# Kernel tuning notes

Measured on AMD Instinct MI355X. Metric: run time of the kernel, lower is better.

Reference implementation:

```python
import jax, jax.numpy as jnp
import numpy as np

N, E, G = 50000, 300000, 64
VOCAB, EMB, FEAT = 10000, 64, 8
DIN, DH, EDIM = EMB * FEAT, 256, 6


def _lin(k, fout, fin):
    kw, kb = jax.random.split(k)
    w = jax.random.normal(kw, (fout, fin), jnp.float32) / float(np.sqrt(fin))
    b = jax.random.normal(kb, (fout,), jnp.float32) * 0.01
    return w, b


def setup_inputs() -> dict:
    key = jax.random.key(0)
    ks = jax.random.split(key, 10)
    inp = {
        'x_idx': jax.random.randint(ks[0], (N, FEAT), 0, VOCAB),
        'edge_index': jax.random.randint(ks[1], (2, E), 0, N),
        'edge_attr': jax.random.normal(ks[2], (E, EDIM), jnp.float32),
        'batch': jnp.sort(jax.random.randint(ks[3], (N,), 0, G)),
        'emb_table': jax.random.normal(ks[4], (VOCAB, EMB), jnp.float32) * 0.1,
    }
    # two TransformerConv layers: lin_query/key/value (d_in->DH), lin_edge (EDIM->DH), lin_skip (d_in->DH)
    for li, kbase, din in ((1, ks[5], DIN), (2, ks[6], DH)):
        sub = jax.random.split(kbase, 5)
        for j, (wn, bn, fin) in enumerate([('wq', 'bq', din), ('wk', 'bk', din), ('wv', 'bv', din), ('we', 'be', EDIM), ('ws', 'bs', din)]):
            w, b = _lin(sub[j], DH, fin)
            inp['c%d_%s' % (li, wn)] = w
            inp['c%d_%s' % (li, bn)] = b
    for i, (fout, fin, k) in enumerate([(256, 2 * DH, ks[7]), (128, 256, ks[8]), (1, 128, ks[9])]):
        w, b = _lin(k, fout, fin)
        inp['w%d' % (i + 1)] = w
        inp['b%d' % (i + 1)] = b
    return inp


def _tconv(h, src, dst, edge_attr, wq, bq, wk, bk, wv, bv, we, be, ws, bs):
    # PyG TransformerConv, heads=1, concat=True, root_weight=True, beta=False
    n = h.shape[0]
    q = h @ wq.T + bq                      # [N, DH]
    k = h @ wk.T + bk
    v = h @ wv.T + bv
    e = edge_attr @ we.T + be              # [E, DH]
    ke = k[src] + e                        # key fused with edge features
    logits = jnp.sum(q[dst] * ke, axis=-1) / jnp.sqrt(jnp.float32(DH))  # [E]
    m = jax.ops.segment_max(logits, dst, num_segments=n)
    m = jnp.where(jnp.isfinite(m), m, 0.0)
    a = jnp.exp(logits - m[dst])
    s = jax.ops.segment_sum(a, dst, num_segments=n)
    a = a / s[dst]                         # scatter-softmax over incoming edges
    agg = jax.ops.segment_sum((v[src] + e) * a[:, None], dst, num_segments=n)
    return agg + h @ ws.T + bs             # skip connection (root_weight)


def reference(x_idx, edge_index, edge_attr, batch, emb_table,
              c1_wq, c1_bq, c1_wk, c1_bk, c1_wv, c1_bv, c1_we, c1_be, c1_ws, c1_bs,
              c2_wq, c2_bq, c2_wk, c2_bk, c2_wv, c2_bv, c2_we, c2_be, c2_ws, c2_bs,
              w1, b1, w2, b2, w3, b3):
    x = emb_table[x_idx].reshape(x_idx.shape[0], DIN)  # [N, EMB*FEAT]
    src, dst = edge_index[0], edge_index[1]
    h = jax.nn.relu(_tconv(x, src, dst, edge_attr, c1_wq, c1_bq, c1_wk, c1_bk, c1_wv, c1_bv, c1_we, c1_be, c1_ws, c1_bs))
    h = jax.nn.relu(_tconv(h, src, dst, edge_attr, c2_wq, c2_bq, c2_wk, c2_bk, c2_wv, c2_bv, c2_we, c2_be, c2_ws, c2_bs))
    cnt = jax.ops.segment_sum(jnp.ones((h.shape[0],), h.dtype), batch, num_segments=G)
    gap = jax.ops.segment_sum(h, batch, num_segments=G) / jnp.maximum(cnt, 1.0)[:, None]
    gmp = jax.ops.segment_max(h, batch, num_segments=G)
    gmp = jnp.where(jnp.isfinite(gmp), gmp, 0.0)
    r = jnp.concatenate([gap, gmp], axis=1)             # [G, 2*DH]
    o = jax.nn.relu(r @ w1.T + b1)
    o = jax.nn.relu(o @ w2.T + b2)
    # dropout skipped (eval mode)
    return jax.nn.sigmoid(o @ w3.T + b3)[:, 0]          # [G]
```

## Files before the change

kernel.cpp:

```cpp
#include <hip/hip_runtime.h>

typedef unsigned long long ull;
typedef __bf16 bf16x8 __attribute__((ext_vector_type(8)));
typedef float f32x4 __attribute__((ext_vector_type(4)));

__device__ __forceinline__ float bf2f(unsigned short u) {
  union { unsigned int i; float f; } c; c.i = ((unsigned int)u) << 16; return c.f;
}
__device__ __forceinline__ unsigned short f2bf(float f) {
  union { float f; unsigned int i; } c; c.f = f;
  unsigned int u = c.i;
  u += 0x7fffu + ((u >> 16) & 1u);
  return (unsigned short)(u >> 16);
}

__global__ __launch_bounds__(256) void pack_weights(
    const float* __restrict__ wq, const float* __restrict__ wk,
    const float* __restrict__ wv, const float* __restrict__ ws,
    const float* __restrict__ bq, const float* __restrict__ bk,
    const float* __restrict__ bv, const float* __restrict__ bs,
    unsigned short* __restrict__ Wcat, float* __restrict__ bcat, int logK) {
  int idx = blockIdx.x * 256 + threadIdx.x;
  if (idx < 1024) {
    int rr = idx >> 8, cc = idx & 255;
    const float* bp = (rr == 0) ? bq : (rr == 1) ? bk : (rr == 2) ? bv : bs;
    bcat[idx] = bp[cc];
  }
  int K = 1 << logK;
  if (idx >= (1024 << logK)) return;
  int kj = idx & 7;
  int lane = (idx >> 3) & 63;
  int rg = (idx >> 9) & 3;
  int ksbits = logK - 5;
  int ks = (idx >> 11) & ((1 << ksbits) - 1);
  int colt = idx >> (11 + ksbits);
  int quad = lane >> 4, lm = lane & 15;
  int o = colt * 64 + rg * 16 + lm;
  int k = ks * 32 + quad * 8 + kj;
  int rr = o >> 8, oo = o & 255;
  const float* wp = (rr == 0) ? wq : (rr == 1) ? wk : (rr == 2) ? wv : ws;
  Wcat[idx] = f2bf(wp[oo * K + k]);
}

__global__ __launch_bounds__(256) void embed_gather(
    const int* __restrict__ x_idx, const float* __restrict__ emb,
    unsigned short* __restrict__ xbf, int total) {
  int idx = blockIdx.x * 256 + threadIdx.x;
  if (idx >= total) return;
  int n = idx >> 9, d = idx & 511, f = d >> 6, j = d & 63;
  int vi = x_idx[n * 8 + f];
  int n32 = n >> 5, lm = n & 15, half = (n >> 4) & 1;
  int ks = d >> 5, quad = (d >> 3) & 3, kj = d & 7;
  size_t a = (((size_t)(n32 * 16 + ks)) * 2 + half) * 512 + (quad * 16 + lm) * 8 + kj;
  xbf[a] = f2bf(emb[vi * 64 + j]);
}

__global__ __launch_bounds__(256) void count_dst(const int* __restrict__ dst,
                                                 int* __restrict__ counts, int E_) {
  int i = blockIdx.x * 256 + threadIdx.x;
  if (i < E_) atomicAdd(&counts[dst[i]], 1);
}

__global__ __launch_bounds__(256) void alloc_rows(const int* __restrict__ counts,
                                                  int* __restrict__ row_start,
                                                  int* __restrict__ cursor,
                                                  int* __restrict__ total, int n) {
  int i = blockIdx.x * 256 + threadIdx.x;
  int lane = threadIdx.x & 63;
  int c = (i < n) ? counts[i] : 0;
  int incl = c;
#pragma unroll
  for (int off = 1; off < 64; off <<= 1) {
    int t = __shfl_up(incl, off, 64);
    if (lane >= off) incl += t;
  }
  int base = 0;
  if (lane == 63) base = atomicAdd(total, incl);
  base = __shfl(base, 63, 64);
  int st = base + incl - c;
  if (i < n) { row_start[i] = st; cursor[i] = st; }
}

__global__ __launch_bounds__(256) void scatter_edges(
    const int* __restrict__ dst, const int* __restrict__ srcA,
    const float* __restrict__ eattr, int* __restrict__ cursor,
    int* __restrict__ srcs, int* __restrict__ dsts,
    float* __restrict__ ea_perm, int E_) {
  int i = blockIdx.x * 256 + threadIdx.x;
  if (i >= E_) return;
  int d = dst[i];
  int p = atomicAdd(&cursor[d], 1);
  srcs[p] = srcA[i];
  dsts[p] = d;
  const float* ea = eattr + (size_t)i * 6;
  float* eo = ea_perm + (size_t)p * 6;
  eo[0] = ea[0]; eo[1] = ea[1]; eo[2] = ea[2];
  eo[3] = ea[3]; eo[4] = ea[4]; eo[5] = ea[5];
}

template <int K>
__global__ __launch_bounds__(256) void gemm_qkvs(
    const unsigned short* __restrict__ X, const unsigned short* __restrict__ W,
    const float* __restrict__ bcat,
    unsigned short* __restrict__ qout, unsigned short* __restrict__ kout,
    unsigned short* __restrict__ vout, float* __restrict__ sout,
    int Nn, int nrb) {
  const int l = blockIdx.x;
  const int xcd = l & 7, j = l >> 3;
  const int q = nrb >> 3, r = nrb & 7;
  const int cnt = q + (xcd < r ? 1 : 0);
  const int lrb = j >> 4, colt = j & 15;
  if (lrb >= cnt) return;
  const int m_blk = xcd * q + min(xcd, r) + lrb;

  const int wid = threadIdx.x >> 6;
  const int lane = threadIdx.x & 63;
  const int quad = lane >> 4, lm = lane & 15;
  const int m_base = m_blk * 128 + wid * 32;
  const int n_base = colt * 64;
  const size_t abase = (size_t)(m_blk * 4 + wid) * (K >> 5) * 1024 + lane * 8;
  const size_t bbase = (size_t)colt * (K >> 5) * 2048 + lane * 8;
  f32x4 acc[2][4] = {};
#pragma unroll 4
  for (int ks = 0; ks < (K >> 5); ks++) {
    const unsigned short* ap = X + abase + (size_t)ks * 1024;
    const unsigned short* bp = W + bbase + (size_t)ks * 2048;
    bf16x8 a0 = *(const bf16x8*)(ap);
    bf16x8 a1 = *(const bf16x8*)(ap + 512);
    bf16x8 b0 = *(const bf16x8*)(bp);
    bf16x8 b1 = *(const bf16x8*)(bp + 512);
    bf16x8 b2 = *(const bf16x8*)(bp + 1024);
    bf16x8 b3 = *(const bf16x8*)(bp + 1536);
    acc[0][0] = __builtin_amdgcn_mfma_f32_16x16x32_bf16(a0, b0, acc[0][0], 0, 0, 0);
    acc[0][1] = __builtin_amdgcn_mfma_f32_16x16x32_bf16(a0, b1, acc[0][1], 0, 0, 0);
    acc[0][2] = __builtin_amdgcn_mfma_f32_16x16x32_bf16(a0, b2, acc[0][2], 0, 0, 0);
    acc[0][3] = __builtin_amdgcn_mfma_f32_16x16x32_bf16(a0, b3, acc[0][3], 0, 0, 0);
    acc[1][0] = __builtin_amdgcn_mfma_f32_16x16x32_bf16(a1, b0, acc[1][0], 0, 0, 0);
    acc[1][1] = __builtin_amdgcn_mfma_f32_16x16x32_bf16(a1, b1, acc[1][1], 0, 0, 0);
    acc[1][2] = __builtin_amdgcn_mfma_f32_16x16x32_bf16(a1, b2, acc[1][2], 0, 0, 0);
    acc[1][3] = __builtin_amdgcn_mfma_f32_16x16x32_bf16(a1, b3, acc[1][3], 0, 0, 0);
  }
#pragma unroll
  for (int mi = 0; mi < 2; mi++) {
#pragma unroll
    for (int r2 = 0; r2 < 4; r2++) {
      int row = m_base + mi * 16 + quad * 4 + r2;
      if (row >= Nn) continue;
      size_t rb = (size_t)row * 256;
#pragma unroll
      for (int ni = 0; ni < 4; ni++) {
        int col = n_base + ni * 16 + lm;
        float v = acc[mi][ni][r2] + bcat[col];
        int reg = col >> 8, c = col & 255;
        if (reg == 0)       qout[rb + c] = f2bf(v * 0.0625f);
        else if (reg == 1)  kout[rb + c] = f2bf(v);
        else if (reg == 2)  vout[rb + c] = f2bf(v);
        else                sout[rb + c] = v;
      }
    }
  }
}

__global__ __launch_bounds__(256) void node_prep(
    const unsigned short* __restrict__ qv,
    const float* __restrict__ we, const float* __restrict__ be,
    float* __restrict__ zc, int Nn) {
  __shared__ float we_s[1536];
  __shared__ float be_s[256];
  for (int i = threadIdx.x; i < 1536; i += 256) we_s[i] = we[i];
  be_s[threadIdx.x] = be[threadIdx.x];
  __syncthreads();
  int wid = threadIdx.x >> 6, lane = threadIdx.x & 63;
  int n = blockIdx.x * 4 + wid;
  if (n >= Nn) return;
  int j0 = lane * 4;
  ull uq = *(const ull*)(qv + (size_t)n * 256 + j0);
  float q0 = bf2f((unsigned short)uq), q1 = bf2f((unsigned short)(uq >> 16));
  float q2 = bf2f((unsigned short)(uq >> 32)), q3 = bf2f((unsigned short)(uq >> 48));
  float part[7];
#pragma unroll
  for (int t = 0; t < 6; t++) {
    part[t] = we_s[(j0 + 0) * 6 + t] * q0 + we_s[(j0 + 1) * 6 + t] * q1
            + we_s[(j0 + 2) * 6 + t] * q2 + we_s[(j0 + 3) * 6 + t] * q3;
  }
  part[6] = be_s[j0] * q0 + be_s[j0 + 1] * q1 + be_s[j0 + 2] * q2 + be_s[j0 + 3] * q3;
#pragma unroll
  for (int off = 32; off > 0; off >>= 1) {
#pragma unroll
    for (int t = 0; t < 7; t++) part[t] += __shfl_xor(part[t], off, 64);
  }
  if (lane == 0) {
    float* zp = zc + (size_t)n * 8;
#pragma unroll
    for (int t = 0; t < 7; t++) zp[t] = part[t];
    zp[7] = 0.f;
  }
}

__device__ __forceinline__ float dot4(ull uq, ull uk) {
  return bf2f((unsigned short)uq) * bf2f((unsigned short)uk)
       + bf2f((unsigned short)(uq >> 16)) * bf2f((unsigned short)(uk >> 16))
       + bf2f((unsigned short)(uq >> 32)) * bf2f((unsigned short)(uk >> 32))
       + bf2f((unsigned short)(uq >> 48)) * bf2f((unsigned short)(uk >> 48));
}

#define SEL8_I(a, t) ((t)==0?(a)[0]:(t)==1?(a)[1]:(t)==2?(a)[2]:(t)==3?(a)[3]:(t)==4?(a)[4]:(t)==5?(a)[5]:(t)==6?(a)[6]:(a)[7])

__global__ __launch_bounds__(256) void edge_logits(
    const int* __restrict__ srcs, const int* __restrict__ dsts,
    const float* __restrict__ ea_perm,
    const unsigned short* __restrict__ qv, const unsigned short* __restrict__ kv,
    const float* __restrict__ zc, int E_, float* __restrict__ logits) {
  int wid = threadIdx.x >> 6, lane = threadIdx.x & 63;
  int p0 = (blockIdx.x * 4 + wid) * 8;
  if (p0 >= E_) return;
  int j0 = lane * 4;
  int s_[8], d_[8];
  if (p0 + 8 <= E_) {
    int4 sa = *(const int4*)(srcs + p0), sb = *(const int4*)(srcs + p0 + 4);
    int4 da = *(const int4*)(dsts + p0), db = *(const int4*)(dsts + p0 + 4);
    s_[0] = sa.x; s_[1] = sa.y; s_[2] = sa.z; s_[3] = sa.w;
    s_[4] = sb.x; s_[5] = sb.y; s_[6] = sb.z; s_[7] = sb.w;
    d_[0] = da.x; d_[1] = da.y; d_[2] = da.z; d_[3] = da.w;
    d_[4] = db.x; d_[5] = db.y; d_[6] = db.z; d_[7] = db.w;
  } else {
#pragma unroll
    for (int t = 0; t < 8; t++) {
      int pp = min(p0 + t, E_ - 1);
      s_[t] = srcs[pp]; d_[t] = dsts[pp];
    }
  }
  ull uk[8], uq[8];
#pragma unroll
  for (int t = 0; t < 8; t++) uk[t] = *(const ull*)(kv + (size_t)s_[t] * 256 + j0);
#pragma unroll
  for (int t = 0; t < 8; t++) uq[t] = *(const ull*)(qv + (size_t)d_[t] * 256 + j0);
  float pv[8];
#pragma unroll
  for (int t = 0; t < 8; t++) pv[t] = dot4(uq[t], uk[t]);
#pragma unroll
  for (int off = 32; off > 0; off >>= 1) {
#pragma unroll
    for (int t = 0; t < 8; t++) pv[t] += __shfl_xor(pv[t], off, 64);
  }
  if (lane < 8 && p0 + lane < E_) {
    int t = lane;
    int dd = SEL8_I(d_, t);
    float pvt = SEL8_I(pv, t);
    const float* zp = zc + (size_t)dd * 8;
    const float* u = ea_perm + (size_t)(p0 + t) * 6;
    float zd = zp[0] * u[0] + zp[1] * u[1] + zp[2] * u[2]
             + zp[3] * u[3] + zp[4] * u[4] + zp[5] * u[5] + zp[6];
    logits[p0 + t] = pvt + zd;
  }
}

__global__ __launch_bounds__(256) void node_softmax(
    const int* __restrict__ row_start, const int* __restrict__ counts,
    const float* __restrict__ ea_perm,
    float* __restrict__ logits, float* __restrict__ ubar, int Nn) {
  int wid = threadIdx.x >> 6, lane = threadIdx.x & 63;
  int n = blockIdx.x * 4 + wid;
  if (n >= Nn) return;
  int beg = row_start[n], cnt = counts[n];
  if (cnt == 0) return;
  float lm = -INFINITY;
  for (int b = lane; b < cnt; b += 64) lm = fmaxf(lm, logits[beg + b]);
#pragma unroll
  for (int off = 32; off > 0; off >>= 1) lm = fmaxf(lm, __shfl_xor(lm, off, 64));
  float se = 0.f;
  for (int b = lane; b < cnt; b += 64) se += __expf(logits[beg + b] - lm);
#pragma unroll
  for (int off = 32; off > 0; off >>= 1) se += __shfl_xor(se, off, 64);
  float inv = 1.f / se;
  float u0 = 0.f, u1 = 0.f, u2 = 0.f, u3 = 0.f, u4 = 0.f, u5 = 0.f;
  for (int b = lane; b < cnt; b += 64) {
    int p = beg + b;
    float w = __expf(logits[p] - lm) * inv;
    logits[p] = w;
    const float* up = ea_perm + (size_t)p * 6;
    u0 += w * up[0]; u1 += w * up[1]; u2 += w * up[2];
    u3 += w * up[3]; u4 += w * up[4]; u5 += w * up[5];
  }
#pragma unroll
  for (int off = 32; off > 0; off >>= 1) {
    u0 += __shfl_xor(u0, off, 64); u1 += __shfl_xor(u1, off, 64);
    u2 += __shfl_xor(u2, off, 64); u3 += __shfl_xor(u3, off, 64);
    u4 += __shfl_xor(u4, off, 64); u5 += __shfl_xor(u5, off, 64);
  }
  if (lane == 0) {
    float* up = ubar + (size_t)n * 8;
    up[0] = u0; up[1] = u1; up[2] = u2; up[3] = u3; up[4] = u4; up[5] = u5;
  }
}

#define NPW 8
__global__ __launch_bounds__(256) void edge_agg_final(
    const int* __restrict__ srcs, const int* __restrict__ row_start,
    const int* __restrict__ counts, const float* __restrict__ wgt,
    const unsigned short* __restrict__ vv,
    const float* __restrict__ ubar, const float* __restrict__ skipv,
    const float* __restrict__ we, const float* __restrict__ be,
    int Nn, int mode,
    unsigned short* __restrict__ hout, float* __restrict__ h_acc) {
  __shared__ float we_s[1536];
  __shared__ float be_s[256];
  for (int i = threadIdx.x; i < 1536; i += 256) we_s[i] = we[i];
  be_s[threadIdx.x] = be[threadIdx.x];
  __syncthreads();
  int wave = blockIdx.x * 4 + (threadIdx.x >> 6);
  int lane = threadIdx.x & 63;
  int n0 = wave * NPW;
  if (n0 >= Nn) return;
  int n1 = min(n0 + NPW, Nn);
  int j0 = lane * 4;
  for (int n = n0; n < n1; n++) {
    int cnt = counts[n];
    float a0 = 0.f, a1 = 0.f, a2 = 0.f, a3 = 0.f;
    float e[4] = {0.f, 0.f, 0.f, 0.f};
    if (cnt > 0) {
      int beg = row_start[n];
      for (int i0 = 0; i0 < cnt; i0 += 8) {
        int m = cnt - i0; if (m > 8) m = 8;
        float w8[8];
        int s8[8];
#pragma unroll
        for (int t = 0; t < 8; t++) {
          int pp = beg + i0 + ((t < m) ? t : (m - 1));
          w8[t] = (t < m) ? wgt[pp] : 0.f;
          s8[t] = srcs[pp];
        }
        ull uv[8];
#pragma unroll
        for (int t = 0; t < 8; t++)
          uv[t] = *(const ull*)(vv + (size_t)s8[t] * 256 + j0);
#pragma unroll
        for (int t = 0; t < 8; t++) {
          float ww = w8[t];
          a0 += ww * bf2f((unsigned short)uv[t]);
          a1 += ww * bf2f((unsigned short)(uv[t] >> 16));
          a2 += ww * bf2f((unsigned short)(uv[t] >> 32));
          a3 += ww * bf2f((unsigned short)(uv[t] >> 48));
        }
      }
      float4 u0 = *(const float4*)(ubar + (size_t)n * 8);
      float4 u1 = *(const float4*)(ubar + (size_t)n * 8 + 4);
#pragma unroll
      for (int r = 0; r < 4; r++) {
        int d = j0 + r;
        e[r] = be_s[d]
             + we_s[d * 6 + 0] * u0.x + we_s[d * 6 + 1] * u0.y + we_s[d * 6 + 2] * u0.z
             + we_s[d * 6 + 3] * u0.w + we_s[d * 6 + 4] * u1.x + we_s[d * 6 + 5] * u1.y;
      }
    }
    float4 skv = *(const float4*)(skipv + (size_t)n * 256 + j0);
    float h0 = fmaxf(a0 + e[0] + skv.x, 0.f);
    float h1 = fmaxf(a1 + e[1] + skv.y, 0.f);
    float h2 = fmaxf(a2 + e[2] + skv.z, 0.f);
    float h3 = fmaxf(a3 + e[3] + skv.w, 0.f);
    if (mode == 0) {
      ull hv = (ull)f2bf(h0) | ((ull)f2bf(h1) << 16) | ((ull)f2bf(h2) << 32) | ((ull)f2bf(h3) << 48);
      int n32 = n >> 5, lmn = n & 15, halfn = (n >> 4) & 1;
      int ks = lane >> 3, quadc = (lane >> 1) & 3, kjc = (lane & 1) * 4;
      size_t a = (((size_t)(n32 * 8 + ks)) * 2 + halfn) * 512 + (quadc * 16 + lmn) * 8 + kjc;
      *(ull*)(hout + a) = hv;
    } else {
      float4 o; o.x = h0; o.y = h1; o.z = h2; o.w = h3;
      *(float4*)(h_acc + (size_t)n * 256 + j0) = o;
    }
  }
}

__global__ __launch_bounds__(256) void pool_reduce(
    const float* __restrict__ hfin, const int* __restrict__ batch, int Nn,
    float* __restrict__ gap, unsigned int* __restrict__ gmp) {
  int g = blockIdx.x, s = blockIdx.y, t = threadIdx.x;
  __shared__ int st_s, en_s;
  if (t == 0) {
    int lo = 0, hi = Nn;
    while (lo < hi) { int mid = (lo + hi) >> 1; if (batch[mid] < g) lo = mid + 1; else hi = mid; }
    st_s = lo;
    lo = 0; hi = Nn;
    while (lo < hi) { int mid = (lo + hi) >> 1; if (batch[mid] < g + 1) lo = mid + 1; else hi = mid; }
    en_s = lo;
  }
  __syncthreads();
  int st = st_s, en = en_s;
  int len = en - st;
  if (len <= 0) return;
  int nsplit = gridDim.y;
  int chunk = (len + nsplit - 1) / nsplit;
  int a = st + s * chunk;
  int b = min(a + chunk, en);
  if (a >= b) return;
  float acc = 0.f, mx = 0.f;
  for (int n = a; n < b; n++) {
    float v = hfin[(size_t)n * 256 + t];
    acc += v;
    mx = fmaxf(mx, v);
  }
  atomicAdd(&gap[(size_t)g * 256 + t], acc);
  atomicMax(&gmp[(size_t)g * 256 + t], __float_as_uint(mx));
}

__global__ __launch_bounds__(256) void pool_mlp(
    const float* __restrict__ gap, const unsigned int* __restrict__ gmp,
    const int* __restrict__ batch, int Nn,
    const float* __restrict__ w1, const float* __restrict__ b1,
    const float* __restrict__ w2, const float* __restrict__ b2,
    const float* __restrict__ w3, const float* __restrict__ b3,
    float* __restrict__ out) {
  int g = blockIdx.x, t = threadIdx.x;
  __shared__ float r[512];
  __shared__ float o1[256];
  __shared__ float o2[128];
  __shared__ float red[256];
  __shared__ int cnt_s;
  if (t == 0) {
    int lo = 0, hi = Nn;
    while (lo < hi) { int mid = (lo + hi) >> 1; if (batch[mid] < g) lo = mid + 1; else hi = mid; }
    int st = lo;
    lo = 0; hi = Nn;
    while (lo < hi) { int mid = (lo + hi) >> 1; if (batch[mid] < g + 1) lo = mid + 1; else hi = mid; }
    cnt_s = lo - st;
  }
  __syncthreads();
  float inv = 1.f / fmaxf((float)cnt_s, 1.f);
  r[t] = gap[(size_t)g * 256 + t] * inv;
  r[256 + t] = __uint_as_float(gmp[(size_t)g * 256 + t]);
  __syncthreads();
  {
    float a = b1[t];
    const float* wr = w1 + (size_t)t * 512;
    for (int k = 0; k < 512; k++) a += wr[k] * r[k];
    o1[t] = fmaxf(a, 0.f);
  }
  __syncthreads();
  if (t < 128) {
    float a = b2[t];
    const float* wr = w2 + (size_t)t * 256;
    for (int k = 0; k < 256; k++) a += wr[k] * o1[k];
    o2[t] = fmaxf(a, 0.f);
  }
  __syncthreads();
  red[t] = (t < 128) ? w3[t] * o2[t] : 0.f;
  __syncthreads();
  for (int s = 128; s > 0; s >>= 1) {
    if (t < s) red[t] += red[t + s];
    __syncthreads();
  }
  if (t == 0) out[g] = 1.f / (1.f + expf(-(red[0] + b3[0])));
}

extern "C" void kernel_launch(void* const* d_in, const int* in_sizes, int n_in,
                              void* d_out, int out_size, void* d_ws, size_t ws_size,
                              hipStream_t stream) {
  const int* x_idx      = (const int*)d_in[0];
  const int* edge_index = (const int*)d_in[1];
  const float* eattr    = (const float*)d_in[2];
  const int* batch      = (const int*)d_in[3];
  const float* emb      = (const float*)d_in[4];
  const float* c1_wq = (const float*)d_in[5],  *c1_bq = (const float*)d_in[6];
  const float* c1_wk = (const float*)d_in[7],  *c1_bk = (const float*)d_in[8];
  const float* c1_wv = (const float*)d_in[9],  *c1_bv = (const float*)d_in[10];
  const float* c1_we = (const float*)d_in[11], *c1_be = (const float*)d_in[12];
  const float* c1_ws = (const float*)d_in[13], *c1_bs = (const float*)d_in[14];
  const float* c2_wq = (const float*)d_in[15], *c2_bq = (const float*)d_in[16];
  const float* c2_wk = (const float*)d_in[17], *c2_bk = (const float*)d_in[18];
  const float* c2_wv = (const float*)d_in[19], *c2_bv = (const float*)d_in[20];
  const float* c2_we = (const float*)d_in[21], *c2_be = (const float*)d_in[22];
  const float* c2_ws = (const float*)d_in[23], *c2_bs = (const float*)d_in[24];
  const float* w1 = (const float*)d_in[25], *b1 = (const float*)d_in[26];
  const float* w2 = (const float*)d_in[27], *b2 = (const float*)d_in[28];
  const float* w3 = (const float*)d_in[29], *b3 = (const float*)d_in[30];

  const int Nn = in_sizes[3];
  const int Ee = in_sizes[1] / 2;
  const int nrb = (Nn + 127) / 128;

  char* ws = (char*)d_ws;
  size_t off = 0;
  auto alloc = [&](size_t bytes) -> void* {
    void* p = ws + off;
    off += (bytes + 255) & ~(size_t)255;
    return p;
  };
  unsigned short* xbf   = (unsigned short*)alloc((size_t)nrb * 128 * 512 * 2);
  unsigned short* qbf   = (unsigned short*)alloc((size_t)Nn * 256 * 2);
  unsigned short* kbf   = (unsigned short*)alloc((size_t)Nn * 256 * 2);
  unsigned short* vbf   = (unsigned short*)alloc((size_t)Nn * 256 * 2);
  float*          skipf = (float*)alloc((size_t)Nn * 256 * 4);
  unsigned short* h1bf  = (unsigned short*)alloc((size_t)nrb * 128 * 256 * 2);
  unsigned short* Wcat1 = (unsigned short*)alloc((size_t)1024 * 512 * 2);
  float*          bcat1 = (float*)alloc(1024 * 4);
  unsigned short* Wcat2 = (unsigned short*)alloc((size_t)1024 * 256 * 2);
  float*          bcat2 = (float*)alloc(1024 * 4);
  int*            counts    = (int*)alloc((size_t)Nn * 4);
  int*            row_start = (int*)alloc((size_t)Nn * 4);
  int*            cursor    = (int*)alloc((size_t)Nn * 4);
  int*            srcs      = (int*)alloc((size_t)Ee * 4);
  int*            dsts      = (int*)alloc((size_t)Ee * 4);
  float*          ea_perm   = (float*)alloc((size_t)Ee * 6 * 4);
  float*          logits    = (float*)alloc((size_t)Ee * 4);
  float*          zc        = (float*)alloc((size_t)Nn * 8 * 4);
  float*          ubar      = (float*)alloc((size_t)Nn * 8 * 4);
  int*            total     = (int*)alloc(256);
  float*          gap       = (float*)alloc((size_t)64 * 256 * 4);
  unsigned int*   gmp       = (unsigned int*)alloc((size_t)64 * 256 * 4);
  float* h_acc = (float*)xbf;

  const int* srcA = edge_index;
  const int* dstA = edge_index + Ee;

  hipMemsetAsync(counts, 0, (size_t)Nn * 4, stream);
  hipMemsetAsync(total, 0, 4, stream);
  hipMemsetAsync(gap, 0, (size_t)64 * 256 * 4, stream);
  hipMemsetAsync(gmp, 0, (size_t)64 * 256 * 4, stream);

  pack_weights<<<(1024 * 512 + 255) / 256, 256, 0, stream>>>(
      c1_wq, c1_wk, c1_wv, c1_ws, c1_bq, c1_bk, c1_bv, c1_bs, Wcat1, bcat1, 9);
  pack_weights<<<(1024 * 256 + 255) / 256, 256, 0, stream>>>(
      c2_wq, c2_wk, c2_wv, c2_ws, c2_bq, c2_bk, c2_bv, c2_bs, Wcat2, bcat2, 8);
  embed_gather<<<((Nn * 512) + 255) / 256, 256, 0, stream>>>(x_idx, emb, xbf, Nn * 512);
  count_dst<<<(Ee + 255) / 256, 256, 0, stream>>>(dstA, counts, Ee);
  alloc_rows<<<(Nn + 255) / 256, 256, 0, stream>>>(counts, row_start, cursor, total, Nn);
  scatter_edges<<<(Ee + 255) / 256, 256, 0, stream>>>(dstA, srcA, eattr, cursor,
                                                      srcs, dsts, ea_perm, Ee);

  const int rbmax = nrb / 8 + ((nrb % 8) ? 1 : 0);
  const int ggrid = 8 * rbmax * 16;
  const int egrid = (Ee + 31) / 32;
  const int sgrid = (Nn + NPW * 4 - 1) / (NPW * 4);
  const int ngrid = (Nn + 3) / 4;

  gemm_qkvs<512><<<ggrid, 256, 0, stream>>>(xbf, Wcat1, bcat1, qbf, kbf, vbf,
                                            skipf, Nn, nrb);
  node_prep<<<ngrid, 256, 0, stream>>>(qbf, c1_we, c1_be, zc, Nn);
  edge_logits<<<egrid, 256, 0, stream>>>(srcs, dsts, ea_perm, qbf, kbf, zc, Ee, logits);
  node_softmax<<<ngrid, 256, 0, stream>>>(row_start, counts, ea_perm, logits, ubar, Nn);
  edge_agg_final<<<sgrid, 256, 0, stream>>>(srcs, row_start, counts, logits, vbf,
                                            ubar, skipf, c1_we, c1_be, Nn, 0,
                                            h1bf, nullptr);

  gemm_qkvs<256><<<ggrid, 256, 0, stream>>>(h1bf, Wcat2, bcat2, qbf, kbf, vbf,
                                            skipf, Nn, nrb);
  node_prep<<<ngrid, 256, 0, stream>>>(qbf, c2_we, c2_be, zc, Nn);
  edge_logits<<<egrid, 256, 0, stream>>>(srcs, dsts, ea_perm, qbf, kbf, zc, Ee, logits);
  node_softmax<<<ngrid, 256, 0, stream>>>(row_start, counts, ea_perm, logits, ubar, Nn);
  edge_agg_final<<<sgrid, 256, 0, stream>>>(srcs, row_start, counts, logits, vbf,
                                            ubar, skipf, c2_we, c2_be, Nn, 1,
                                            nullptr, h_acc);

  dim3 pg(64, 16);
  pool_reduce<<<pg, 256, 0, stream>>>(h_acc, batch, Nn, gap, gmp);
  pool_mlp<<<64, 256, 0, stream>>>(gap, gmp, batch, Nn, w1, b1, w2, b2, w3, b3,
                                   (float*)d_out);
}
```

Before: 768.8 us.

## Stage GEMM weight tiles in double-buffered LDS shared by all waves

The QKVS projection GEMM now loads each weight tile into a double-buffered shared-memory buffer once per block, instead of having each of the four waves read it from global memory separately. The load of the next chunk of four k-steps is issued before the MFMAs on the current chunk and written to the other buffer afterwards, so global loads overlap with compute. This cuts redundant global and L2 traffic for the weight operand. In exchange it adds 32 KB of LDS per block, which may lower occupancy, plus a block-wide barrier per chunk. The activation operand is still read straight from global memory.

```diff
diff --git a/kernel.cpp b/kernel.cpp
--- a/kernel.cpp
+++ b/kernel.cpp
@@ -105,6 +105,7 @@
     unsigned short* __restrict__ qout, unsigned short* __restrict__ kout,
     unsigned short* __restrict__ vout, float* __restrict__ sout,
     int Nn, int nrb) {
+  __shared__ unsigned short Bs[2][8192];
   const int l = blockIdx.x;
   const int xcd = l & 7, j = l >> 3;
   const int q = nrb >> 3, r = nrb & 7;
@@ -113,32 +114,68 @@
   if (lrb >= cnt) return;
   const int m_blk = xcd * q + min(xcd, r) + lrb;
 
-  const int wid = threadIdx.x >> 6;
-  const int lane = threadIdx.x & 63;
+  const int tid = threadIdx.x;
+  const int wid = tid >> 6;
+  const int lane = tid & 63;
   const int quad = lane >> 4, lm = lane & 15;
   const int m_base = m_blk * 128 + wid * 32;
   const int n_base = colt * 64;
   const size_t abase = (size_t)(m_blk * 4 + wid) * (K >> 5) * 1024 + lane * 8;
-  const size_t bbase = (size_t)colt * (K >> 5) * 2048 + lane * 8;
+  const unsigned short* wchunk = W + (size_t)colt * (K >> 5) * 2048;
+  const int nc = (K >> 5) / 4;
   f32x4 acc[2][4] = {};
-#pragma unroll 4
-  for (int ks = 0; ks < (K >> 5); ks++) {
-    const unsigned short* ap = X + abase + (size_t)ks * 1024;
-    const unsigned short* bp = W + bbase + (size_t)ks * 2048;
-    bf16x8 a0 = *(const bf16x8*)(ap);
-    bf16x8 a1 = *(const bf16x8*)(ap + 512);
-    bf16x8 b0 = *(const bf16x8*)(bp);
-    bf16x8 b1 = *(const bf16x8*)(bp + 512);
-    bf16x8 b2 = *(const bf16x8*)(bp + 1024);
-    bf16x8 b3 = *(const bf16x8*)(bp + 1536);
-    acc[0][0] = __builtin_amdgcn_mfma_f32_16x16x32_bf16(a0, b0, acc[0][0], 0, 0, 0);
-    acc[0][1] = __builtin_amdgcn_mfma_f32_16x16x32_bf16(a0, b1, acc[0][1], 0, 0, 0);
-    acc[0][2] = __builtin_amdgcn_mfma_f32_16x16x32_bf16(a0, b2, acc[0][2], 0, 0, 0);
-    acc[0][3] = __builtin_amdgcn_mfma_f32_16x16x32_bf16(a0, b3, acc[0][3], 0, 0, 0);
-    acc[1][0] = __builtin_amdgcn_mfma_f32_16x16x32_bf16(a1, b0, acc[1][0], 0, 0, 0);
-    acc[1][1] = __builtin_amdgcn_mfma_f32_16x16x32_bf16(a1, b1, acc[1][1], 0, 0, 0);
-    acc[1][2] = __builtin_amdgcn_mfma_f32_16x16x32_bf16(a1, b2, acc[1][2], 0, 0, 0);
-    acc[1][3] = __builtin_amdgcn_mfma_f32_16x16x32_bf16(a1, b3, acc[1][3], 0, 0, 0);
+
+  {
+    bf16x8 st0 = *(const bf16x8*)(wchunk + 0 * 2048 + tid * 8);
+    bf16x8 st1 = *(const bf16x8*)(wchunk + 1 * 2048 + tid * 8);
+    bf16x8 st2 = *(const bf16x8*)(wchunk + 2 * 2048 + tid * 8);
+    bf16x8 st3 = *(const bf16x8*)(wchunk + 3 * 2048 + tid * 8);
+    *(bf16x8*)(&Bs[0][0 * 2048 + tid * 8]) = st0;
+    *(bf16x8*)(&Bs[0][1 * 2048 + tid * 8]) = st1;
+    *(bf16x8*)(&Bs[0][2 * 2048 + tid * 8]) = st2;
+    *(bf16x8*)(&Bs[0][3 * 2048 + tid * 8]) = st3;
+  }
+  __syncthreads();
+
+  for (int c = 0; c < nc; c++) {
+    bf16x8 st0, st1, st2, st3;
+    const bool pf = (c + 1 < nc);
+    if (pf) {
+      const unsigned short* wp = wchunk + (size_t)(c + 1) * 8192;
+      st0 = *(const bf16x8*)(wp + 0 * 2048 + tid * 8);
+      st1 = *(const bf16x8*)(wp + 1 * 2048 + tid * 8);
+      st2 = *(const bf16x8*)(wp + 2 * 2048 + tid * 8);
+      st3 = *(const bf16x8*)(wp + 3 * 2048 + tid * 8);
+    }
+    const unsigned short* bs = &Bs[c & 1][0];
+#pragma unroll
+    for (int s = 0; s < 4; s++) {
+      const int ks = c * 4 + s;
+      const unsigned short* ap = X + abase + (size_t)ks * 1024;
+      const unsigned short* bp = bs + s * 2048 + lane * 8;
+      bf16x8 a0 = *(const bf16x8*)(ap);
+      bf16x8 a1 = *(const bf16x8*)(ap + 512);
+      bf16x8 b0 = *(const bf16x8*)(bp);
+      bf16x8 b1 = *(const bf16x8*)(bp + 512);
+      bf16x8 b2 = *(const bf16x8*)(bp + 1024);
+      bf16x8 b3 = *(const bf16x8*)(bp + 1536);
+      acc[0][0] = __builtin_amdgcn_mfma_f32_16x16x32_bf16(a0, b0, acc[0][0], 0, 0, 0);
+      acc[0][1] = __builtin_amdgcn_mfma_f32_16x16x32_bf16(a0, b1, acc[0][1], 0, 0, 0);
+      acc[0][2] = __builtin_amdgcn_mfma_f32_16x16x32_bf16(a0, b2, acc[0][2], 0, 0, 0);
+      acc[0][3] = __builtin_amdgcn_mfma_f32_16x16x32_bf16(a0, b3, acc[0][3], 0, 0, 0);
+      acc[1][0] = __builtin_amdgcn_mfma_f32_16x16x32_bf16(a1, b0, acc[1][0], 0, 0, 0);
+      acc[1][1] = __builtin_amdgcn_mfma_f32_16x16x32_bf16(a1, b1, acc[1][1], 0, 0, 0);
+      acc[1][2] = __builtin_amdgcn_mfma_f32_16x16x32_bf16(a1, b2, acc[1][2], 0, 0, 0);
+      acc[1][3] = __builtin_amdgcn_mfma_f32_16x16x32_bf16(a1, b3, acc[1][3], 0, 0, 0);
+    }
+    if (pf) {
+      unsigned short* bw = &Bs[(c + 1) & 1][0];
+      *(bf16x8*)(bw + 0 * 2048 + tid * 8) = st0;
+      *(bf16x8*)(bw + 1 * 2048 + tid * 8) = st1;
+      *(bf16x8*)(bw + 2 * 2048 + tid * 8) = st2;
+      *(bf16x8*)(bw + 3 * 2048 + tid * 8) = st3;
+    }
+    __syncthreads();
   }
 #pragma unroll
   for (int mi = 0; mi < 2; mi++) {
@@ -151,11 +188,11 @@
       for (int ni = 0; ni < 4; ni++) {
         int col = n_base + ni * 16 + lm;
         float v = acc[mi][ni][r2] + bcat[col];
-        int reg = col >> 8, c = col & 255;
-        if (reg == 0)       qout[rb + c] = f2bf(v * 0.0625f);
-        else if (reg == 1)  kout[rb + c] = f2bf(v);
-        else if (reg == 2)  vout[rb + c] = f2bf(v);
-        else                sout[rb + c] = v;
+        int reg = col >> 8, c2 = col & 255;
+        if (reg == 0)       qout[rb + c2] = f2bf(v * 0.0625f);
+        else if (reg == 1)  kout[rb + c2] = f2bf(v);
+        else if (reg == 2)  vout[rb + c2] = f2bf(v);
+        else                sout[rb + c2] = v;
       }
     }
   }
```

Result: no change. 754.8 us (-1.8%).
